# Kernel optimization log

Measured on AMD Instinct MI355X. Metric: run time of the kernel, lower is better.

The kernel has to match this reference:

```python
import jax, jax.numpy as jnp
import numpy as np

B, T, D = 2, 2048, 1024
NH, NKV, HD = 16, 4, 64
BASE, TSL, QGI = 10000.0, 1024, 1.5
EPS = 1.1920929e-07  # torch.finfo(float32).eps used by F.rms_norm default


def _rope_cos_sin(seq_len, rd):
    # Rotary.forward with self.rd == head_dim (Attn sets rd=0 -> full rotation)
    if seq_len > TSL:  # NTK-style base rescale branch
        nb = BASE * (seq_len / TSL) ** (rd / (rd - 2))
    else:
        nb = BASE
    inv = 1.0 / nb ** (jnp.arange(0, rd, 2, dtype=jnp.float32) / rd)
    fr = jnp.arange(seq_len, dtype=jnp.float32)[:, None] * inv[None, :]
    return jnp.cos(fr)[None, :, None, :], jnp.sin(fr)[None, :, None, :]


def _apply_rope(x, cos, sin):
    h = x.shape[-1] // 2
    x1, x2 = x[..., :h], x[..., h:]
    return jnp.concatenate([x1 * cos + x2 * sin, -x1 * sin + x2 * cos], axis=-1)


def _rms_norm(x):
    return x * jax.lax.rsqrt(jnp.mean(x * x, axis=-1, keepdims=True) + EPS)


def setup_inputs() -> dict:
    key = jax.random.key(0)
    ks = jax.random.split(key, 8)
    s = jnp.float32(0.02)
    return {
        "x": jax.random.normal(ks[0], (B, T, D), jnp.float32),
        "qw": jax.random.normal(ks[1], (NH * HD, D), jnp.float32) * s,
        "kw": jax.random.normal(ks[2], (NKV * HD, D), jnp.float32) * s,
        "vw": jax.random.normal(ks[3], (NKV * HD, D), jnp.float32) * s,
        "ow": jax.random.normal(ks[4], (D, D), jnp.float32) * s,
        "ve": jax.random.normal(ks[5], (B, T, NKV * HD), jnp.float32) * s,
        "v0": jax.random.normal(ks[6], (B, T, NKV, HD), jnp.float32) * s,
        "q_gain": jnp.full((NH,), QGI, jnp.float32),
        "vr_lambda": jnp.array([0.5, 0.5], jnp.float32),
        "gate_w": jnp.zeros((NH, D), jnp.float32),      # nn.init.zeros_
        "gate_b": jnp.full((NH,), 4.0, jnp.float32),    # nn.init.constant_(4.0)
    }


def reference(x, qw, kw, vw, ow, ve, v0, q_gain, vr_lambda, gate_w, gate_b):
    # projections
    q = (x @ qw.T).reshape(B, T, NH, HD)
    k = (x @ kw.T).reshape(B, T, NKV, HD)
    v = (x @ vw.T + ve).reshape(B, T, NKV, HD)
    raw_v = v  # returned when vr=True
    v = vr_lambda[0] * v0 + vr_lambda[1] * v  # value residual
    # qk rms-norm + rope (full head dim since self.rd == 0) + per-head q gain
    q = _rms_norm(q)
    k = _rms_norm(k)
    cos, sin = _rope_cos_sin(T, HD)
    q = _apply_rope(q, cos, sin)
    k = _apply_rope(k, cos, sin)
    q = q * q_gain[None, None, :, None]
    # causal GQA attention (nh query heads share nkv kv heads)
    G = NH // NKV
    qg = q.reshape(B, T, NKV, G, HD)
    scale = 1.0 / np.sqrt(HD).astype(np.float32)
    scores = jnp.einsum('bqhgd,bkhd->bhgqk', qg, k) * scale  # [B,NKV,G,T,T]
    causal = jnp.tril(jnp.ones((T, T), bool))
    scores = jnp.where(causal[None, None, None], scores, jnp.finfo(scores.dtype).min)
    p = jax.nn.softmax(scores, axis=-1)
    y = jnp.einsum('bhgqk,bkhd->bqhgd', p, v).reshape(B, T, NH, HD)
    # gated attention output
    gate = jax.nn.sigmoid(x @ gate_w.T + gate_b)  # [B,T,NH]
    y = y * gate[..., None]
    out = y.reshape(B, T, D) @ ow.T
    return out, raw_v
```

## Files before the change

kernel.cpp:

```cpp
#include <hip/hip_runtime.h>
#include <math.h>

#define BB 2
#define TT 2048
#define DD 1024
#define NH 16
#define NKV 4
#define HD 64
#define EPSF 1.1920929e-07f
#define LOG2_NB 14.319970444065578
#define SCALE_LOG2E 0.18033688011112042f
#define FIXMAX 17.5f

typedef __attribute__((ext_vector_type(8))) short bf16x8;
typedef __attribute__((ext_vector_type(4))) float f32x4;

__device__ inline short f2bf(float f) {
    unsigned u = __builtin_bit_cast(unsigned, f);
    unsigned r = (u + 0x7fffu + ((u >> 16) & 1u)) >> 16;
    return (short)r;
}
__device__ inline unsigned cvt_pk_bf16(float a, float b) {
    unsigned r;
    asm("v_cvt_pk_bf16_f32 %0, %1, %2" : "=v"(r) : "v"(a), "v"(b));
    return r;
}

__global__ __launch_bounds__(256) void conv_all(
    const float* __restrict__ x, const float* __restrict__ qw,
    const float* __restrict__ kw, const float* __restrict__ vw,
    const float* __restrict__ ow,
    short* __restrict__ x16, short* __restrict__ wb16, short* __restrict__ ow16)
{
    int i = blockIdx.x * 256 + threadIdx.x;
    const float* src; short* dst; int j;
    if (i < 1048576)      { src = x;  dst = x16;            j = i; }
    else if (i < 1310720) { src = qw; dst = wb16;           j = i - 1048576; }
    else if (i < 1376256) { src = kw; dst = wb16 + 1048576; j = i - 1310720; }
    else if (i < 1441792) { src = vw; dst = wb16 + 1310720; j = i - 1376256; }
    else                  { src = ow; dst = ow16;           j = i - 1441792; }
    float4 v = ((const float4*)src)[j];
    short4 o;
    o.x = f2bf(v.x); o.y = f2bf(v.y); o.z = f2bf(v.z); o.w = f2bf(v.w);
    ((short4*)dst)[j] = o;
}

__global__ __launch_bounds__(256, 4) void gemm_mfma(
    const short* __restrict__ A, const short* __restrict__ Bmat,
    float* __restrict__ C, int ldc, int klen)
{
    __shared__ short As[2][128*32];
    __shared__ short Bs[2][128*32];
    int tid = threadIdx.x;
    int w = tid >> 6, lane = tid & 63;
    int quad = lane >> 4, lc = lane & 15;
    int wy = w >> 1, wx = w & 1;
    int m0 = blockIdx.y * 128, n0 = blockIdx.x * 128;
    int kbeg = blockIdx.z * klen, kend = kbeg + klen;
    float* Cz = C + (size_t)blockIdx.z * 4096 * ldc;

    f32x4 acc[4][4];
    #pragma unroll
    for (int i = 0; i < 4; i++)
        #pragma unroll
        for (int j = 0; j < 4; j++) acc[i][j] = (f32x4){0.f,0.f,0.f,0.f};

    #define GSTAGE(buf, k0)                                                             \
    {                                                                                   \
        _Pragma("unroll")                                                               \
        for (int i = 0; i < 2; i++) {                                                   \
            int off = w*2048 + i*1024;                   \
            int g = (off >> 4) + lane;                               \
            int row = g >> 2, c = g & 3;                                                \
            int cg = c ^ (row & 3);                                    \
            const short* ga = A + (size_t)(m0 + row)*1024 + (k0) + cg*8;                \
            __builtin_amdgcn_global_load_lds(                                           \
                (const __attribute__((address_space(1))) void*)ga,                      \
                (__attribute__((address_space(3))) void*)((char*)&As[buf][0] + off), 16, 0, 0); \
            const short* gb = Bmat + (size_t)(n0 + row)*1024 + (k0) + cg*8;             \
            __builtin_amdgcn_global_load_lds(                                           \
                (const __attribute__((address_space(1))) void*)gb,                      \
                (__attribute__((address_space(3))) void*)((char*)&Bs[buf][0] + off), 16, 0, 0); \
        }                                                                               \
    }

    GSTAGE(0, kbeg);
    __syncthreads();

    for (int k0 = kbeg; k0 < kend; k0 += 32) {
        int cur = ((k0 - kbeg) >> 5) & 1;

        bf16x8 af[4], bfr[4];
        #pragma unroll
        for (int tm = 0; tm < 4; tm++) {
            int row = wy*64 + tm*16 + lc;
            af[tm] = *(const bf16x8*)(&As[cur][0] + row*32 + ((quad*8) ^ ((row&3)*8)));
        }
        #pragma unroll
        for (int tn = 0; tn < 4; tn++) {
            int row = wx*64 + tn*16 + lc;
            bfr[tn] = *(const bf16x8*)(&Bs[cur][0] + row*32 + ((quad*8) ^ ((row&3)*8)));
        }
        if (k0 + 32 < kend) GSTAGE(cur ^ 1, k0 + 32);
        #pragma unroll
        for (int tm = 0; tm < 4; tm++)
            #pragma unroll
            for (int tn = 0; tn < 4; tn++)
                acc[tm][tn] = __builtin_amdgcn_mfma_f32_16x16x32_bf16(af[tm], bfr[tn], acc[tm][tn], 0, 0, 0);
        __syncthreads();
    }

    #pragma unroll
    for (int tm = 0; tm < 4; tm++)
        #pragma unroll
        for (int r = 0; r < 4; r++) {
            int m = m0 + wy*64 + tm*16 + quad*4 + r;
            #pragma unroll
            for (int tn = 0; tn < 4; tn++) {
                int n = n0 + wx*64 + tn*16 + lc;
                Cz[(size_t)m*ldc + n] = acc[tm][tn][r];
            }
        }
}

__global__ __launch_bounds__(256) void qkv_epilogue(
    const float* __restrict__ qp0, const float* __restrict__ qp1,
    const float* __restrict__ ve, const float* __restrict__ v0,
    const float* __restrict__ q_gain, const float* __restrict__ vr_lambda,
    short* __restrict__ qbh, short* __restrict__ kbh, short* __restrict__ vb,
    float* __restrict__ rawv)
{
    int wave = blockIdx.x * 4 + (threadIdx.x >> 6);
    int lane = threadIdx.x & 63;
    int row = wave / 24;
    int hh  = wave % 24;
    int b = row >> 11;
    int t = row & (TT - 1);

    if (hh < 20) {
        int col = (hh < 16) ? (hh*64 + lane) : (1024 + (hh-16)*64 + lane);
        size_t idx = (size_t)row*1536 + col;
        float val = qp0[idx] + qp1[idx];
        float ss = val * val;
        #pragma unroll
        for (int off = 32; off; off >>= 1) ss += __shfl_xor(ss, off);
        val *= rsqrtf(ss * (1.0f/64.0f) + EPSF);
        float partner = __shfl(val, lane ^ 32);
        int idxr = lane & 31;
        float inv = (float)exp2((double)idxr * (-LOG2_NB / 32.0));
        float fr = (float)t * inv;
        float sn, cs;
        sincosf(fr, &sn, &cs);
        float outv = (lane < 32) ? (val*cs + partner*sn) : (val*cs - partner*sn);
        if (hh < 16) {
            outv *= q_gain[hh] * SCALE_LOG2E;
            qbh[(((size_t)(b*16 + hh))*2048 + t)*64 + lane] = f2bf(outv);
        } else {
            kbh[(((size_t)(b*4 + (hh-16)))*2048 + t)*64 + lane] = f2bf(outv);
        }
    } else {
        int vh = hh - 20;
        size_t off = ((size_t)row*4 + vh)*64 + lane;
        size_t idx = (size_t)row*1536 + 1280 + vh*64 + lane;
        float vraw = qp0[idx] + qp1[idx] + ve[off];
        rawv[off] = vraw;
        float vmix = vr_lambda[0]*v0[off] + vr_lambda[1]*vraw;
        vb[off] = f2bf(vmix);
    }
}

__global__ __launch_bounds__(256) void transpose_v(
    const short* __restrict__ vb, short* __restrict__ vtb)
{
    __shared__ short tile[64][72];
    int bk = blockIdx.x;
    int tt = blockIdx.y;
    int b = bk >> 2, kvh = bk & 3;
    int tid = threadIdx.x;
    int t4 = tid >> 4;
    int d4 = (tid & 15) * 4;
    #pragma unroll
    for (int i = 0; i < 4; i++) {
        int t = t4 + i*16;
        const short* src = vb + (((size_t)(b*2048 + tt*64 + t)*4 + kvh)*64 + d4);
        *(short4*)&tile[t][d4] = *(const short4*)src;
    }
    __syncthreads();
    #pragma unroll
    for (int i = 0; i < 4; i++) {
        int d = t4 + i*16;
        int t0 = d4;
        short4 o;
        o.x = tile[t0+0][d]; o.y = tile[t0+1][d];
        o.z = tile[t0+2][d]; o.w = tile[t0+3][d];
        *(short4*)&vtb[((size_t)(bk*64 + d))*2048 + tt*64 + t0] = o;
    }
}

__global__ __launch_bounds__(256) void gate_kernel(
    const float* __restrict__ x, const float* __restrict__ gw,
    const float* __restrict__ gb, float* __restrict__ gate)
{
    __shared__ float xs[1024];
    int row = blockIdx.x;
    int tid = threadIdx.x;
    *(float4*)&xs[tid*4] = *(const float4*)&x[(size_t)row*1024 + tid*4];
    __syncthreads();
    int wave = tid >> 6, lane = tid & 63;
    for (int h = wave; h < 16; h += 4) {
        const float* w = gw + (size_t)h * 1024;
        float s = 0.f;
        #pragma unroll
        for (int i = 0; i < 16; i++) s += xs[lane + 64*i] * w[lane + 64*i];
        #pragma unroll
        for (int off = 32; off; off >>= 1) s += __shfl_xor(s, off);
        if (lane == 0) gate[(size_t)row*16 + h] = 1.0f / (1.0f + __expf(-(s + gb[h])));
    }
}

__global__ __launch_bounds__(256, 4) void flash_mfma(
    const short* __restrict__ qbh, const short* __restrict__ kbh,
    const short* __restrict__ vtb, const float* __restrict__ gate,
    short* __restrict__ y16)
{
    __shared__ short Ks[2][64*64];
    __shared__ short Vt[2][64*64];
    __shared__ short Ps[4][16*64];

    int bh = blockIdx.x;
    int b = bh >> 4, h = bh & 15, kvh = h >> 2;
    int qt = 31 - blockIdx.y;
    int tid = threadIdx.x;
    int w = tid >> 6, lane = tid & 63;
    int quad = lane >> 4, lc = lane & 15;

    const short* qbase = qbh + (((size_t)bh)*2048 + qt*64 + w*16 + lc)*64;
    bf16x8 qf0 = *(const bf16x8*)(qbase + quad*8);
    bf16x8 qf1 = *(const bf16x8*)(qbase + 32 + quad*8);

    f32x4 o[4];
    #pragma unroll
    for (int i = 0; i < 4; i++) o[i] = (f32x4){0.f,0.f,0.f,0.f};
    f32x4 l4 = (f32x4){0.f,0.f,0.f,0.f};
    const bf16x8 ones = {(short)0x3F80,(short)0x3F80,(short)0x3F80,(short)0x3F80,
                         (short)0x3F80,(short)0x3F80,(short)0x3F80,(short)0x3F80};

    const size_t kbase = ((size_t)(b*4 + kvh))*2048*64;
    const size_t vbase = ((size_t)(b*4 + kvh))*64*2048;

    #define STAGE(buf, kt)                                                              \
    {                                                                                   \
        _Pragma("unroll")                                                               \
        for (int i = 0; i < 2; i++) {                                                   \
            int off = w*2048 + i*1024;                                                  \
            int g = (off >> 4) + lane;                                                  \
            int row = g >> 3, c = g & 7;                                                \
            int cg = c ^ (row & 7);                                                     \
            const short* gk = kbh + kbase + (size_t)((kt)*64 + row)*64 + cg*8;          \
            __builtin_amdgcn_global_load_lds(                                           \
                (const __attribute__((address_space(1))) void*)gk,                      \
                (__attribute__((address_space(3))) void*)((char*)Ks[buf] + off), 16, 0, 0); \
            const short* gv = vtb + vbase + (size_t)row*2048 + (kt)*64 + cg*8;          \
            __builtin_amdgcn_global_load_lds(                                           \
                (const __attribute__((address_space(1))) void*)gv,                      \
                (__attribute__((address_space(3))) void*)((char*)Vt[buf] + off), 16, 0, 0); \
        }                                                                               \
    }

    STAGE(0, 0);
    __syncthreads();

    short* ps = Ps[w];

    for (int kt = 0; kt <= qt; kt++) {
        int cur = kt & 1;
        bool diag = (kt == qt);

        bf16x8 kf0[4], kf1[4], vf0[4], vf1[4];
        #pragma unroll
        for (int kn = 0; kn < 4; kn++) {
            int row = kn*16 + lc;
            int sw = (row & 7) * 8;
            const short* kr = Ks[cur] + row*64;
            kf0[kn] = *(const bf16x8*)(kr + ((quad*8) ^ sw));
            kf1[kn] = *(const bf16x8*)(kr + ((quad*8 + 32) ^ sw));
            const short* vr = Vt[cur] + row*64;
            vf0[kn] = *(const bf16x8*)(vr + ((quad*8) ^ sw));
            vf1[kn] = *(const bf16x8*)(vr + ((quad*8 + 32) ^ sw));
        }
        if (kt < qt) STAGE(cur ^ 1, kt + 1);

        f32x4 s4[4];
        #pragma unroll
        for (int kn = 0; kn < 4; kn++) {
            f32x4 acc = (f32x4){0.f,0.f,0.f,0.f};
            acc = __builtin_amdgcn_mfma_f32_16x16x32_bf16(kf0[kn], qf0, acc, 0, 0, 0);
            acc = __builtin_amdgcn_mfma_f32_16x16x32_bf16(kf1[kn], qf1, acc, 0, 0, 0);
            s4[kn] = acc;
        }

        #pragma unroll
        for (int kn = 0; kn < 4; kn++) {
            float p0 = __builtin_amdgcn_exp2f(s4[kn][0] - FIXMAX);
            float p1 = __builtin_amdgcn_exp2f(s4[kn][1] - FIXMAX);
            float p2 = __builtin_amdgcn_exp2f(s4[kn][2] - FIXMAX);
            float p3 = __builtin_amdgcn_exp2f(s4[kn][3] - FIXMAX);
            if (diag) {
                int keyb = kn*16 + quad*4, qv = w*16 + lc;
                if (keyb + 0 > qv) p0 = 0.f;
                if (keyb + 1 > qv) p1 = 0.f;
                if (keyb + 2 > qv) p2 = 0.f;
                if (keyb + 3 > qv) p3 = 0.f;
            }
            int c = kn*4 + quad;
            int cs = c ^ ((lc & 7) << 1);
            int2 pk;
            pk.x = (int)cvt_pk_bf16(p0, p1);
            pk.y = (int)cvt_pk_bf16(p2, p3);
            *(int2*)(ps + lc*64 + cs*4) = pk;
        }
        __asm__ volatile("s_waitcnt lgkmcnt(0)" ::: "memory");
        int u0 = (0*4 + quad) ^ (lc & 7);
        int u1 = (1*4 + quad) ^ (lc & 7);
        bf16x8 pf0 = *(const bf16x8*)(ps + lc*64 + u0*8);
        bf16x8 pf1 = *(const bf16x8*)(ps + lc*64 + u1*8);

        #pragma unroll
        for (int dn = 0; dn < 4; dn++) {
            o[dn] = __builtin_amdgcn_mfma_f32_16x16x32_bf16(pf0, vf0[dn], o[dn], 0, 0, 0);
            o[dn] = __builtin_amdgcn_mfma_f32_16x16x32_bf16(pf1, vf1[dn], o[dn], 0, 0, 0);
        }
        l4 = __builtin_amdgcn_mfma_f32_16x16x32_bf16(pf0, ones, l4, 0, 0, 0);
        l4 = __builtin_amdgcn_mfma_f32_16x16x32_bf16(pf1, ones, l4, 0, 0, 0);
        __syncthreads();
    }

    #pragma unroll
    for (int r = 0; r < 4; r++) {
        int row = b*2048 + qt*64 + w*16 + quad*4 + r;
        float g = gate[(size_t)row*16 + h] / l4[r];
        #pragma unroll
        for (int dn = 0; dn < 4; dn++)
            y16[(size_t)row*1024 + h*64 + dn*16 + lc] = f2bf(o[dn][r] * g);
    }
}

extern "C" void kernel_launch(void* const* d_in, const int* in_sizes, int n_in,
                              void* d_out, int out_size, void* d_ws, size_t ws_size,
                              hipStream_t stream) {
    (void)in_sizes; (void)n_in; (void)out_size; (void)ws_size;
    const float* x  = (const float*)d_in[0];
    const float* qw = (const float*)d_in[1];
    const float* kw = (const float*)d_in[2];
    const float* vw = (const float*)d_in[3];
    const float* ow = (const float*)d_in[4];
    const float* ve = (const float*)d_in[5];
    const float* v0 = (const float*)d_in[6];
    const float* qg = (const float*)d_in[7];
    const float* vl = (const float*)d_in[8];
    const float* gw = (const float*)d_in[9];
    const float* gb = (const float*)d_in[10];

    float* out  = (float*)d_out;
    float* rawv = out + (size_t)BB*TT*DD;

    float* ws   = (float*)d_ws;
    float* qkvp = ws;
    float* p    = ws + 2*6291456;
    short* x16  = (short*)p;        p += 2097152;
    short* wb16 = (short*)p;        p += 786432;
    short* ow16 = (short*)p;        p += 524288;
    short* qbh  = (short*)p;        p += 2097152;
    short* kbh  = (short*)p;        p += 524288;
    short* vtb  = (short*)p;        p += 524288;
    short* vb   = (short*)p;        p += 524288;
    float* gt   = p;
    short* y16  = (short*)qkvp;

    conv_all<<<6656, 256, 0, stream>>>(x, qw, kw, vw, ow, x16, wb16, ow16);
    gemm_mfma<<<dim3(12, 32, 2), 256, 0, stream>>>(x16, wb16, qkvp, 1536, 512);
    qkv_epilogue<<<24576, 256, 0, stream>>>(qkvp, qkvp + 6291456, ve, v0, qg, vl,
                                            qbh, kbh, vb, rawv);
    transpose_v<<<dim3(8, 32), 256, 0, stream>>>(vb, vtb);
    gate_kernel<<<4096, 256, 0, stream>>>(x, gw, gb, gt);
    flash_mfma<<<dim3(32, 32), 256, 0, stream>>>(qbh, kbh, vtb, gt, y16);
    gemm_mfma<<<dim3(8, 32, 1), 256, 0, stream>>>(y16, ow16, out, 1024, 1024);
}
```

Baseline: 210.4 us.

## Enlarge flash query tile, fuse x conversion into gate, add narrow out-GEMM, hardware sincos

The flash attention kernel now gives each block 128 query rows, so every K/V tile loaded into shared memory serves two 16-row query groups per wave. Waves whose rows lie entirely before a key tile skip its compute, and occupancy is lowered to two blocks per CU. The bf16 conversion of x moves into the gate kernel, removing a separate pass over x. The output projection uses a new 128x64-tile GEMM that launches more blocks, and RoPE sin/cos switches to v_sin/v_cos on a range-reduced argument, which may lose some accuracy.

```diff
diff --git a/kernel.cpp b/kernel.cpp
--- a/kernel.cpp
+++ b/kernel.cpp
@@ -11,6 +11,7 @@
 #define LOG2_NB 14.319970444065578
 #define SCALE_LOG2E 0.18033688011112042f
 #define FIXMAX 17.5f
+#define INV2PI 0.15915494309189535f
 
 typedef __attribute__((ext_vector_type(8))) short bf16x8;
 typedef __attribute__((ext_vector_type(4))) float f32x4;
@@ -25,20 +26,24 @@
     asm("v_cvt_pk_bf16_f32 %0, %1, %2" : "=v"(r) : "v"(a), "v"(b));
     return r;
 }
-
-__global__ __launch_bounds__(256) void conv_all(
-    const float* __restrict__ x, const float* __restrict__ qw,
-    const float* __restrict__ kw, const float* __restrict__ vw,
-    const float* __restrict__ ow,
-    short* __restrict__ x16, short* __restrict__ wb16, short* __restrict__ ow16)
+__device__ inline float hw_sin(float rev) {
+    float r; asm("v_sin_f32 %0, %1" : "=v"(r) : "v"(rev)); return r;
+}
+__device__ inline float hw_cos(float rev) {
+    float r; asm("v_cos_f32 %0, %1" : "=v"(r) : "v"(rev)); return r;
+}
+
+__global__ __launch_bounds__(256) void conv_w(
+    const float* __restrict__ qw, const float* __restrict__ kw,
+    const float* __restrict__ vw, const float* __restrict__ ow,
+    short* __restrict__ wb16, short* __restrict__ ow16)
 {
     int i = blockIdx.x * 256 + threadIdx.x;
     const float* src; short* dst; int j;
-    if (i < 1048576)      { src = x;  dst = x16;            j = i; }
-    else if (i < 1310720) { src = qw; dst = wb16;           j = i - 1048576; }
-    else if (i < 1376256) { src = kw; dst = wb16 + 1048576; j = i - 1310720; }
-    else if (i < 1441792) { src = vw; dst = wb16 + 1310720; j = i - 1376256; }
-    else                  { src = ow; dst = ow16;           j = i - 1441792; }
+    if (i < 262144)      { src = qw; dst = wb16;           j = i; }
+    else if (i < 327680) { src = kw; dst = wb16 + 1048576; j = i - 262144; }
+    else if (i < 393216) { src = vw; dst = wb16 + 1310720; j = i - 327680; }
+    else                 { src = ow; dst = ow16;           j = i - 393216; }
     float4 v = ((const float4*)src)[j];
     short4 o;
     o.x = f2bf(v.x); o.y = f2bf(v.y); o.z = f2bf(v.z); o.w = f2bf(v.w);
@@ -89,7 +94,6 @@
 
     for (int k0 = kbeg; k0 < kend; k0 += 32) {
         int cur = ((k0 - kbeg) >> 5) & 1;
-
         bf16x8 af[4], bfr[4];
         #pragma unroll
         for (int tm = 0; tm < 4; tm++) {
@@ -120,6 +124,83 @@
                 int n = n0 + wx*64 + tn*16 + lc;
                 Cz[(size_t)m*ldc + n] = acc[tm][tn][r];
             }
+        }
+}
+
+__global__ __launch_bounds__(256, 4) void gemm_out_mfma(
+    const short* __restrict__ A, const short* __restrict__ Bmat, float* __restrict__ C)
+{
+    __shared__ short As[2][128*32];
+    __shared__ short Bs[2][64*32];
+    int tid = threadIdx.x;
+    int w = tid >> 6, lane = tid & 63;
+    int quad = lane >> 4, lc = lane & 15;
+    int m0 = blockIdx.y * 128, n0 = blockIdx.x * 64;
+
+    f32x4 acc[2][4];
+    #pragma unroll
+    for (int i = 0; i < 2; i++)
+        #pragma unroll
+        for (int j = 0; j < 4; j++) acc[i][j] = (f32x4){0.f,0.f,0.f,0.f};
+
+    #define OSTAGE(buf, k0)                                                             \
+    {                                                                                   \
+        _Pragma("unroll")                                                               \
+        for (int i = 0; i < 2; i++) {                                                   \
+            int off = w*2048 + i*1024;                                                  \
+            int g = (off >> 4) + lane;                                                  \
+            int row = g >> 2, c = g & 3;                                                \
+            int cg = c ^ (row & 3);                                                     \
+            const short* ga = A + (size_t)(m0 + row)*1024 + (k0) + cg*8;                \
+            __builtin_amdgcn_global_load_lds(                                           \
+                (const __attribute__((address_space(1))) void*)ga,                      \
+                (__attribute__((address_space(3))) void*)((char*)&As[buf][0] + off), 16, 0, 0); \
+        }                                                                               \
+        {                                                                               \
+            int off = w*1024;                                                           \
+            int g = (off >> 4) + lane;                                                  \
+            int row = g >> 2, c = g & 3;                                                \
+            int cg = c ^ (row & 3);                                                     \
+            const short* gb = Bmat + (size_t)(n0 + row)*1024 + (k0) + cg*8;             \
+            __builtin_amdgcn_global_load_lds(                                           \
+                (const __attribute__((address_space(1))) void*)gb,                      \
+                (__attribute__((address_space(3))) void*)((char*)&Bs[buf][0] + off), 16, 0, 0); \
+        }                                                                               \
+    }
+
+    OSTAGE(0, 0);
+    __syncthreads();
+
+    for (int k0 = 0; k0 < 1024; k0 += 32) {
+        int cur = (k0 >> 5) & 1;
+        bf16x8 af[2], bfr[4];
+        #pragma unroll
+        for (int tm = 0; tm < 2; tm++) {
+            int row = w*32 + tm*16 + lc;
+            af[tm] = *(const bf16x8*)(&As[cur][0] + row*32 + ((quad*8) ^ ((row&3)*8)));
+        }
+        #pragma unroll
+        for (int tn = 0; tn < 4; tn++) {
+            int row = tn*16 + lc;
+            bfr[tn] = *(const bf16x8*)(&Bs[cur][0] + row*32 + ((quad*8) ^ ((row&3)*8)));
+        }
+        if (k0 + 32 < 1024) OSTAGE(cur ^ 1, k0 + 32);
+        #pragma unroll
+        for (int tm = 0; tm < 2; tm++)
+            #pragma unroll
+            for (int tn = 0; tn < 4; tn++)
+                acc[tm][tn] = __builtin_amdgcn_mfma_f32_16x16x32_bf16(af[tm], bfr[tn], acc[tm][tn], 0, 0, 0);
+        __syncthreads();
+    }
+
+    #pragma unroll
+    for (int tm = 0; tm < 2; tm++)
+        #pragma unroll
+        for (int r = 0; r < 4; r++) {
+            int m = m0 + w*32 + tm*16 + quad*4 + r;
+            #pragma unroll
+            for (int tn = 0; tn < 4; tn++)
+                C[(size_t)m*1024 + n0 + tn*16 + lc] = acc[tm][tn][r];
         }
 }
 
@@ -149,8 +230,9 @@
         int idxr = lane & 31;
         float inv = (float)exp2((double)idxr * (-LOG2_NB / 32.0));
         float fr = (float)t * inv;
-        float sn, cs;
-        sincosf(fr, &sn, &cs);
+        float rev = fr * INV2PI;
+        rev = rev - floorf(rev);
+        float sn = hw_sin(rev), cs = hw_cos(rev);
         float outv = (lane < 32) ? (val*cs + partner*sn) : (val*cs - partner*sn);
         if (hh < 16) {
             outv *= q_gain[hh] * SCALE_LOG2E;
@@ -199,12 +281,16 @@
 
 __global__ __launch_bounds__(256) void gate_kernel(
     const float* __restrict__ x, const float* __restrict__ gw,
-    const float* __restrict__ gb, float* __restrict__ gate)
+    const float* __restrict__ gb, float* __restrict__ gate, short* __restrict__ x16)
 {
     __shared__ float xs[1024];
     int row = blockIdx.x;
     int tid = threadIdx.x;
-    *(float4*)&xs[tid*4] = *(const float4*)&x[(size_t)row*1024 + tid*4];
+    float4 xv = *(const float4*)&x[(size_t)row*1024 + tid*4];
+    *(float4*)&xs[tid*4] = xv;
+    short4 xo;
+    xo.x = f2bf(xv.x); xo.y = f2bf(xv.y); xo.z = f2bf(xv.z); xo.w = f2bf(xv.w);
+    ((short4*)(x16 + (size_t)row*1024))[tid] = xo;
     __syncthreads();
     int wave = tid >> 6, lane = tid & 63;
     for (int h = wave; h < 16; h += 4) {
@@ -218,30 +304,38 @@
     }
 }
 
-__global__ __launch_bounds__(256, 4) void flash_mfma(
+__global__ __launch_bounds__(256, 2) void flash_mfma(
     const short* __restrict__ qbh, const short* __restrict__ kbh,
     const short* __restrict__ vtb, const float* __restrict__ gate,
     short* __restrict__ y16)
 {
     __shared__ short Ks[2][64*64];
     __shared__ short Vt[2][64*64];
-    __shared__ short Ps[4][16*64];
+    __shared__ short Ps[4][32*64];
 
     int bh = blockIdx.x;
     int b = bh >> 4, h = bh & 15, kvh = h >> 2;
-    int qt = 31 - blockIdx.y;
+    int qt = 15 - blockIdx.y;
     int tid = threadIdx.x;
     int w = tid >> 6, lane = tid & 63;
     int quad = lane >> 4, lc = lane & 15;
 
-    const short* qbase = qbh + (((size_t)bh)*2048 + qt*64 + w*16 + lc)*64;
-    bf16x8 qf0 = *(const bf16x8*)(qbase + quad*8);
-    bf16x8 qf1 = *(const bf16x8*)(qbase + 32 + quad*8);
-
-    f32x4 o[4];
-    #pragma unroll
-    for (int i = 0; i < 4; i++) o[i] = (f32x4){0.f,0.f,0.f,0.f};
-    f32x4 l4 = (f32x4){0.f,0.f,0.f,0.f};
+    bf16x8 qf[2][2];
+    #pragma unroll
+    for (int qg = 0; qg < 2; qg++) {
+        const short* qbase = qbh + (((size_t)bh)*2048 + qt*128 + w*32 + qg*16 + lc)*64;
+        qf[qg][0] = *(const bf16x8*)(qbase + quad*8);
+        qf[qg][1] = *(const bf16x8*)(qbase + 32 + quad*8);
+    }
+
+    f32x4 o[2][4];
+    f32x4 l4[2];
+    #pragma unroll
+    for (int qg = 0; qg < 2; qg++) {
+        l4[qg] = (f32x4){0.f,0.f,0.f,0.f};
+        #pragma unroll
+        for (int i = 0; i < 4; i++) o[qg][i] = (f32x4){0.f,0.f,0.f,0.f};
+    }
     const bf16x8 ones = {(short)0x3F80,(short)0x3F80,(short)0x3F80,(short)0x3F80,
                          (short)0x3F80,(short)0x3F80,(short)0x3F80,(short)0x3F80};
 
@@ -271,78 +365,92 @@
     __syncthreads();
 
     short* ps = Ps[w];
-
-    for (int kt = 0; kt <= qt; kt++) {
+    int nkt = 2*qt + 2;
+    int qmax_w = qt*128 + w*32 + 31;
+
+    for (int kt = 0; kt < nkt; kt++) {
         int cur = kt & 1;
-        bool diag = (kt == qt);
+        bool live = (kt*64 <= qmax_w);
 
         bf16x8 kf0[4], kf1[4], vf0[4], vf1[4];
-        #pragma unroll
-        for (int kn = 0; kn < 4; kn++) {
-            int row = kn*16 + lc;
-            int sw = (row & 7) * 8;
-            const short* kr = Ks[cur] + row*64;
-            kf0[kn] = *(const bf16x8*)(kr + ((quad*8) ^ sw));
-            kf1[kn] = *(const bf16x8*)(kr + ((quad*8 + 32) ^ sw));
-            const short* vr = Vt[cur] + row*64;
-            vf0[kn] = *(const bf16x8*)(vr + ((quad*8) ^ sw));
-            vf1[kn] = *(const bf16x8*)(vr + ((quad*8 + 32) ^ sw));
-        }
-        if (kt < qt) STAGE(cur ^ 1, kt + 1);
-
-        f32x4 s4[4];
-        #pragma unroll
-        for (int kn = 0; kn < 4; kn++) {
-            f32x4 acc = (f32x4){0.f,0.f,0.f,0.f};
-            acc = __builtin_amdgcn_mfma_f32_16x16x32_bf16(kf0[kn], qf0, acc, 0, 0, 0);
-            acc = __builtin_amdgcn_mfma_f32_16x16x32_bf16(kf1[kn], qf1, acc, 0, 0, 0);
-            s4[kn] = acc;
-        }
-
-        #pragma unroll
-        for (int kn = 0; kn < 4; kn++) {
-            float p0 = __builtin_amdgcn_exp2f(s4[kn][0] - FIXMAX);
-            float p1 = __builtin_amdgcn_exp2f(s4[kn][1] - FIXMAX);
-            float p2 = __builtin_amdgcn_exp2f(s4[kn][2] - FIXMAX);
-            float p3 = __builtin_amdgcn_exp2f(s4[kn][3] - FIXMAX);
-            if (diag) {
-                int keyb = kn*16 + quad*4, qv = w*16 + lc;
-                if (keyb + 0 > qv) p0 = 0.f;
-                if (keyb + 1 > qv) p1 = 0.f;
-                if (keyb + 2 > qv) p2 = 0.f;
-                if (keyb + 3 > qv) p3 = 0.f;
+        if (live) {
+            #pragma unroll
+            for (int kn = 0; kn < 4; kn++) {
+                int row = kn*16 + lc;
+                int sw = (row & 7) * 8;
+                const short* kr = Ks[cur] + row*64;
+                kf0[kn] = *(const bf16x8*)(kr + ((quad*8) ^ sw));
+                kf1[kn] = *(const bf16x8*)(kr + ((quad*8 + 32) ^ sw));
+                const short* vr = Vt[cur] + row*64;
+                vf0[kn] = *(const bf16x8*)(vr + ((quad*8) ^ sw));
+                vf1[kn] = *(const bf16x8*)(vr + ((quad*8 + 32) ^ sw));
             }
-            int c = kn*4 + quad;
-            int cs = c ^ ((lc & 7) << 1);
-            int2 pk;
-            pk.x = (int)cvt_pk_bf16(p0, p1);
-            pk.y = (int)cvt_pk_bf16(p2, p3);
-            *(int2*)(ps + lc*64 + cs*4) = pk;
-        }
-        __asm__ volatile("s_waitcnt lgkmcnt(0)" ::: "memory");
-        int u0 = (0*4 + quad) ^ (lc & 7);
-        int u1 = (1*4 + quad) ^ (lc & 7);
-        bf16x8 pf0 = *(const bf16x8*)(ps + lc*64 + u0*8);
-        bf16x8 pf1 = *(const bf16x8*)(ps + lc*64 + u1*8);
-
-        #pragma unroll
-        for (int dn = 0; dn < 4; dn++) {
-            o[dn] = __builtin_amdgcn_mfma_f32_16x16x32_bf16(pf0, vf0[dn], o[dn], 0, 0, 0);
-            o[dn] = __builtin_amdgcn_mfma_f32_16x16x32_bf16(pf1, vf1[dn], o[dn], 0, 0, 0);
-        }
-        l4 = __builtin_amdgcn_mfma_f32_16x16x32_bf16(pf0, ones, l4, 0, 0, 0);
-        l4 = __builtin_amdgcn_mfma_f32_16x16x32_bf16(pf1, ones, l4, 0, 0, 0);
+        }
+        if (kt + 1 < nkt) STAGE(cur ^ 1, kt + 1);
+
+        if (live) {
+            #pragma unroll
+            for (int qg = 0; qg < 2; qg++) {
+                f32x4 s4[4];
+                #pragma unroll
+                for (int kn = 0; kn < 4; kn++) {
+                    f32x4 acc = (f32x4){0.f,0.f,0.f,0.f};
+                    acc = __builtin_amdgcn_mfma_f32_16x16x32_bf16(kf0[kn], qf[qg][0], acc, 0, 0, 0);
+                    acc = __builtin_amdgcn_mfma_f32_16x16x32_bf16(kf1[kn], qf[qg][1], acc, 0, 0, 0);
+                    s4[kn] = acc;
+                }
+                bool diag = (kt*64 + 63 > qt*128 + w*32 + qg*16);
+                int qv = qt*128 + w*32 + qg*16 + lc;
+                #pragma unroll
+                for (int kn = 0; kn < 4; kn++) {
+                    float p0 = __builtin_amdgcn_exp2f(s4[kn][0] - FIXMAX);
+                    float p1 = __builtin_amdgcn_exp2f(s4[kn][1] - FIXMAX);
+                    float p2 = __builtin_amdgcn_exp2f(s4[kn][2] - FIXMAX);
+                    float p3 = __builtin_amdgcn_exp2f(s4[kn][3] - FIXMAX);
+                    if (diag) {
+                        int keyb = kt*64 + kn*16 + quad*4;
+                        if (keyb + 0 > qv) p0 = 0.f;
+                        if (keyb + 1 > qv) p1 = 0.f;
+                        if (keyb + 2 > qv) p2 = 0.f;
+                        if (keyb + 3 > qv) p3 = 0.f;
+                    }
+                    int c = kn*4 + quad;
+                    int cs = c ^ ((lc & 7) << 1);
+                    int2 pk;
+                    pk.x = (int)cvt_pk_bf16(p0, p1);
+                    pk.y = (int)cvt_pk_bf16(p2, p3);
+                    *(int2*)(ps + (qg*16 + lc)*64 + cs*4) = pk;
+                }
+            }
+            __asm__ volatile("s_waitcnt lgkmcnt(0)" ::: "memory");
+            #pragma unroll
+            for (int qg = 0; qg < 2; qg++) {
+                int u0 = quad ^ (lc & 7);
+                int u1 = (4 + quad) ^ (lc & 7);
+                bf16x8 pf0 = *(const bf16x8*)(ps + (qg*16 + lc)*64 + u0*8);
+                bf16x8 pf1 = *(const bf16x8*)(ps + (qg*16 + lc)*64 + u1*8);
+                #pragma unroll
+                for (int dn = 0; dn < 4; dn++) {
+                    o[qg][dn] = __builtin_amdgcn_mfma_f32_16x16x32_bf16(pf0, vf0[dn], o[qg][dn], 0, 0, 0);
+                    o[qg][dn] = __builtin_amdgcn_mfma_f32_16x16x32_bf16(pf1, vf1[dn], o[qg][dn], 0, 0, 0);
+                }
+                l4[qg] = __builtin_amdgcn_mfma_f32_16x16x32_bf16(pf0, ones, l4[qg], 0, 0, 0);
+                l4[qg] = __builtin_amdgcn_mfma_f32_16x16x32_bf16(pf1, ones, l4[qg], 0, 0, 0);
+            }
+        }
         __syncthreads();
     }
 
     #pragma unroll
-    for (int r = 0; r < 4; r++) {
-        int row = b*2048 + qt*64 + w*16 + quad*4 + r;
-        float g = gate[(size_t)row*16 + h] / l4[r];
-        #pragma unroll
-        for (int dn = 0; dn < 4; dn++)
-            y16[(size_t)row*1024 + h*64 + dn*16 + lc] = f2bf(o[dn][r] * g);
-    }
+    for (int qg = 0; qg < 2; qg++)
+        #pragma unroll
+        for (int r = 0; r < 4; r++) {
+            int row = b*2048 + qt*128 + w*32 + qg*16 + quad*4 + r;
+            float g = gate[(size_t)row*16 + h] / l4[qg][r];
+            #pragma unroll
+            for (int dn = 0; dn < 4; dn++)
+                y16[(size_t)row*1024 + h*64 + dn*16 + lc] = f2bf(o[qg][dn][r] * g);
+        }
 }
 
 extern "C" void kernel_launch(void* const* d_in, const int* in_sizes, int n_in,
@@ -377,12 +485,12 @@
     float* gt   = p;
     short* y16  = (short*)qkvp;
 
-    conv_all<<<6656, 256, 0, stream>>>(x, qw, kw, vw, ow, x16, wb16, ow16);
+    conv_w<<<2560, 256, 0, stream>>>(qw, kw, vw, ow, wb16, ow16);
+    gate_kernel<<<4096, 256, 0, stream>>>(x, gw, gb, gt, x16);
     gemm_mfma<<<dim3(12, 32, 2), 256, 0, stream>>>(x16, wb16, qkvp, 1536, 512);
     qkv_epilogue<<<24576, 256, 0, stream>>>(qkvp, qkvp + 6291456, ve, v0, qg, vl,
                                             qbh, kbh, vb, rawv);
     transpose_v<<<dim3(8, 32), 256, 0, stream>>>(vb, vtb);
-    gate_kernel<<<4096, 256, 0, stream>>>(x, gw, gb, gt);
-    flash_mfma<<<dim3(32, 32), 256, 0, stream>>>(qbh, kbh, vtb, gt, y16);
-    gemm_mfma<<<dim3(8, 32, 1), 256, 0, stream>>>(y16, ow16, out, 1024, 1024);
-}
+    flash_mfma<<<dim3(32, 16), 256, 0, stream>>>(qbh, kbh, vtb, gt, y16);
+    gemm_out_mfma<<<dim3(16, 32), 256, 0, stream>>>(y16, ow16, out);
+}
```

Result: no change. 212.2 us (+0.9%).
